# Performance work log

Measured on AMD Instinct MI355X. Metric: run time of the kernel, lower is better.

## Reference

```python
import jax, jax.numpy as jnp
import numpy as np

BETA = 0.5
N = 4096

def setup_inputs() -> dict:
    key = jax.random.key(0)
    k1, k2, k3 = jax.random.split(key, 3)
    A = jax.random.uniform(k1, (N, N), dtype=jnp.float32)
    h = jax.random.normal(k2, (N, N), dtype=jnp.float32)
    W = jax.random.normal(k3, (N, N), dtype=jnp.float32) * (1.0 / np.sqrt(N))
    return {"A": A, "h": h, "W": W}

def reference(A, h, W):
    # degrees from original A (before self-loops); D = diag(deg) + I is diagonal,
    # so torch.inverse(D) == elementwise reciprocal 1/(deg+1)
    deg = jnp.sum(A, axis=1)                       # [N]
    inv_d = 1.0 / (deg + 1.0)                      # [N]
    A_I = A + jnp.eye(A.shape[0], dtype=A.dtype)   # A += I
    # A_st = (A+I) @ diag(inv_d): scale columns
    A_st = A_I * inv_d[None, :]                    # [N,N]
    # A_st_11 = A_st @ h is dead code in the original (never used) -> skipped
    temp = BETA * h + (1.0 - BETA) * A_st          # [N,N]
    return temp @ W                                # [N,N]
```

## Files before the change

### kernel.cpp

```cpp
#include <hip/hip_runtime.h>
#include <hip/hip_bf16.h>

typedef unsigned short u16;
typedef unsigned int u32;
typedef __attribute__((ext_vector_type(8))) short bf16x8;
typedef __attribute__((ext_vector_type(4))) short s16x4;
typedef __attribute__((ext_vector_type(4))) float f32x4;

#define NN 4096

__device__ __forceinline__ u16 f2bf(float f) {
    union { float f; u32 u; } v; v.f = f;
    u32 r = v.u + 0x7fffu + ((v.u >> 16) & 1u);
    return (u16)(r >> 16);
}

__global__ void rowsum_kernel(const float* __restrict__ A, float* __restrict__ invd) {
    const int row = blockIdx.x;
    const float4* a4 = reinterpret_cast<const float4*>(A + (size_t)row * NN);
    float s = 0.f;
    #pragma unroll
    for (int i = 0; i < 4; ++i) {
        float4 v = a4[threadIdx.x + i * 256];
        s += v.x + v.y + v.z + v.w;
    }
    #pragma unroll
    for (int off = 32; off > 0; off >>= 1) s += __shfl_down(s, off, 64);
    __shared__ float ws[4];
    if ((threadIdx.x & 63) == 0) ws[threadIdx.x >> 6] = s;
    __syncthreads();
    if (threadIdx.x == 0) {
        float t = ws[0] + ws[1] + ws[2] + ws[3];
        invd[row] = 1.0f / (t + 1.0f);
    }
}

__global__ void make_temp_kernel(const float* __restrict__ A, const float* __restrict__ h,
                                 const float* __restrict__ invd, u16* __restrict__ T) {
    const size_t g = ((size_t)blockIdx.x * 256 + threadIdx.x) * 8;
    const int row = (int)(g >> 12);
    const int col = (int)(g & 4095);
    const float4* a4 = reinterpret_cast<const float4*>(A + g);
    const float4* h4 = reinterpret_cast<const float4*>(h + g);
    const float4* d4 = reinterpret_cast<const float4*>(invd + col);
    float4 a0 = a4[0], a1 = a4[1];
    float4 h0 = h4[0], h1 = h4[1];
    float4 dd0 = d4[0], dd1 = d4[1];
    float av[8] = {a0.x,a0.y,a0.z,a0.w,a1.x,a1.y,a1.z,a1.w};
    float hv[8] = {h0.x,h0.y,h0.z,h0.w,h1.x,h1.y,h1.z,h1.w};
    float dv[8] = {dd0.x,dd0.y,dd0.z,dd0.w,dd1.x,dd1.y,dd1.z,dd1.w};
    bf16x8 o;
    #pragma unroll
    for (int j = 0; j < 8; ++j) {
        float aa = av[j] + ((col + j == row) ? 1.0f : 0.0f);
        float t = 0.5f * hv[j] + 0.5f * aa * dv[j];
        o[j] = (short)f2bf(t);
    }
    *reinterpret_cast<bf16x8*>(T + g) = o;
}

__global__ void transposeW_kernel(const float* __restrict__ W, u16* __restrict__ Wt) {
    __shared__ float tile[64][65];
    const int nt = blockIdx.x & 63;
    const int kt = blockIdx.x >> 6;
    const int k0 = kt * 64, n0 = nt * 64;
    const int tr = threadIdx.x >> 4;
    const int tc = (threadIdx.x & 15) * 4;
    #pragma unroll
    for (int rr = 0; rr < 64; rr += 16) {
        float4 v = *reinterpret_cast<const float4*>(&W[(size_t)(k0 + tr + rr) * NN + n0 + tc]);
        tile[tr + rr][tc + 0] = v.x;
        tile[tr + rr][tc + 1] = v.y;
        tile[tr + rr][tc + 2] = v.z;
        tile[tr + rr][tc + 3] = v.w;
    }
    __syncthreads();
    #pragma unroll
    for (int rr = 0; rr < 64; rr += 16) {
        const int n = tr + rr;
        s16x4 o;
        #pragma unroll
        for (int j = 0; j < 4; ++j) o[j] = (short)f2bf(tile[tc + j][n]);
        *reinterpret_cast<s16x4*>(&Wt[(size_t)(n0 + n) * NN + k0 + tc]) = o;
    }
}


#define GLD16(g, l) __builtin_amdgcn_global_load_lds( \
    (const __attribute__((address_space(1))) void*)(g), \
    (__attribute__((address_space(3))) void*)(l), 16, 0, 0)

__global__ __launch_bounds__(512, 2) void gemm_kernel(
    const u16* __restrict__ Atl,
    const u16* __restrict__ Btl,
    float* __restrict__ C)
{
    __shared__ u16 SA[3][8192];
    __shared__ u16 SB[3][8192];

    const int tid  = threadIdx.x;
    const int wid  = tid >> 6;
    const int lane = tid & 63;
    const int llo  = lane & 15;
    const int lhi  = lane >> 4;
    const int wr   = wid >> 2;
    const int wc   = wid & 3;

    const int swz = ((int)blockIdx.x & 7) * 32 + ((int)blockIdx.x >> 3);
    const int bm = swz >> 4, bn = swz & 15;
    const int tileRow = bm * 256, tileCol = bn * 256;

    const int r0 = tid >> 2;
    const int kc = (((tid & 3) ^ ((r0 >> 1) & 3)) << 3);
    const size_t R128 = (size_t)128 * NN;
    const u16* gA = Atl + (size_t)(tileRow + r0) * NN + kc;
    const u16* gB = Btl + (size_t)(tileCol + r0) * NN + kc;

    #define STAGE(WB, KOFF) do { \
        GLD16(gA + (KOFF),        &SA[WB][tid * 8]); \
        GLD16(gA + R128 + (KOFF), &SA[WB][4096 + tid * 8]); \
        GLD16(gB + (KOFF),        &SB[WB][tid * 8]); \
        GLD16(gB + R128 + (KOFF), &SB[WB][4096 + tid * 8]); } while (0)

    int offA[8], offB[4];
    #pragma unroll
    for (int m = 0; m < 8; ++m) {
        const int row = wr * 128 + m * 16 + llo;
        offA[m] = row * 32 + ((lhi ^ ((row >> 1) & 3)) << 3);
    }
    #pragma unroll
    for (int n = 0; n < 4; ++n) {
        const int row = wc * 64 + n * 16 + llo;
        offB[n] = row * 32 + ((lhi ^ ((row >> 1) & 3)) << 3);
    }

    f32x4 acc[8][4];
    #pragma unroll
    for (int m = 0; m < 8; ++m)
        #pragma unroll
        for (int n = 0; n < 4; ++n)
            acc[m][n] = (f32x4){0.f, 0.f, 0.f, 0.f};

    bf16x8 aE[8], bE[4], aO[8], bO[4];

    STAGE(0, 0);
    STAGE(1, 32);
    asm volatile("s_waitcnt vmcnt(4)" ::: "memory");
    __builtin_amdgcn_s_barrier();
    asm volatile("" ::: "memory");
    #pragma unroll
    for (int m = 0; m < 8; ++m) aE[m] = *reinterpret_cast<const bf16x8*>(&SA[0][0] + offA[m]);
    #pragma unroll
    for (int n = 0; n < 4; ++n) bE[n] = *reinterpret_cast<const bf16x8*>(&SB[0][0] + offB[n]);

    int wb = 2;
    int rb = 1;
    int koff = 64;

    #define STEP(SG, VM0, RD, AC, BC, AN, BN) do { \
        if (SG) { STAGE(wb, koff); koff += 32; } \
        if (VM0) asm volatile("s_waitcnt vmcnt(0)" ::: "memory"); \
        else     asm volatile("s_waitcnt vmcnt(4)" ::: "memory"); \
        __builtin_amdgcn_s_barrier(); \
        asm volatile("" ::: "memory"); \
        const u16* rA = &SA[rb][0]; \
        const u16* rB = &SB[rb][0]; \
        if (RD) { \
            _Pragma("unroll") \
            for (int m = 0; m < 4; ++m) AN[m] = *reinterpret_cast<const bf16x8*>(rA + offA[m]); \
        } \
        __builtin_amdgcn_sched_barrier(0); \
        __builtin_amdgcn_s_setprio(1); \
        _Pragma("unroll") \
        for (int m = 0; m < 4; ++m) \
            _Pragma("unroll") \
            for (int n = 0; n < 4; ++n) \
                acc[m][n] = __builtin_amdgcn_mfma_f32_16x16x32_bf16(AC[m], BC[n], acc[m][n], 0, 0, 0); \
        __builtin_amdgcn_s_setprio(0); \
        __builtin_amdgcn_sched_barrier(0); \
        if (RD) { \
            _Pragma("unroll") \
            for (int m = 4; m < 8; ++m) AN[m] = *reinterpret_cast<const bf16x8*>(rA + offA[m]); \
            _Pragma("unroll") \
            for (int n = 0; n < 4; ++n) BN[n] = *reinterpret_cast<const bf16x8*>(rB + offB[n]); \
        } \
        __builtin_amdgcn_sched_barrier(0); \
        __builtin_amdgcn_s_setprio(1); \
        _Pragma("unroll") \
        for (int m = 4; m < 8; ++m) \
            _Pragma("unroll") \
            for (int n = 0; n < 4; ++n) \
                acc[m][n] = __builtin_amdgcn_mfma_f32_16x16x32_bf16(AC[m], BC[n], acc[m][n], 0, 0, 0); \
        __builtin_amdgcn_s_setprio(0); \
        rb = (rb == 2) ? 0 : rb + 1; \
        wb = (wb == 2) ? 0 : wb + 1; \
    } while (0)

    #pragma unroll 1
    for (int tt = 0; tt < 64; ++tt) {
        const bool sg = tt < 63;
        STEP(sg, !sg, true, aE, bE, aO, bO);
        STEP(sg, !sg && false, sg, aO, bO, aE, bE);
    }
    #undef STEP
    #undef STAGE

    #pragma unroll
    for (int m = 0; m < 8; ++m) {
        #pragma unroll
        for (int n = 0; n < 4; ++n) {
            const size_t rbase = (size_t)(tileRow + wr * 128 + m * 16 + lhi * 4) * NN
                               + tileCol + wc * 64 + n * 16 + llo;
            #pragma unroll
            for (int j = 0; j < 4; ++j)
                C[rbase + (size_t)j * NN] = acc[m][n][j];
        }
    }
}

extern "C" void kernel_launch(void* const* d_in, const int* in_sizes, int n_in,
                              void* d_out, int out_size, void* d_ws, size_t ws_size,
                              hipStream_t stream) {
    const float* A = (const float*)d_in[0];
    const float* h = (const float*)d_in[1];
    const float* W = (const float*)d_in[2];
    float* out = (float*)d_out;

    float* invd = (float*)d_ws;
    u16* temp = (u16*)((char*)d_ws + 16384);
    u16* wt   = temp + (size_t)NN * NN;

    rowsum_kernel<<<NN, 256, 0, stream>>>(A, invd);
    make_temp_kernel<<<(NN * (size_t)NN) / (256 * 8), 256, 0, stream>>>(A, h, invd, temp);
    transposeW_kernel<<<(NN / 64) * (NN / 64), 256, 0, stream>>>(W, wt);
    gemm_kernel<<<256, 512, 0, stream>>>(temp, wt, out);
}
```

Before: 179.0 us.

## Load B fragments directly from global into registers, double-buffer A with K=64 tiles

Restructures the GEMM pipeline. The B operand is no longer staged in LDS; each wave loads its B fragments straight from global memory into registers, double-buffered across steps. The A operand now uses a two-buffer LDS scheme with 64-wide K tiles and an 8-way XOR swizzle. This removes the LDS traffic and space for B and halves the number of barriers, but the A-tile reads from LDS move onto the critical path. It also relies on global-load latency for B, and wave pairs that share columns now fetch the same B data redundantly through cache.

```diff
diff --git a/kernel.cpp b/kernel.cpp
--- a/kernel.cpp
+++ b/kernel.cpp
@@ -90,13 +90,12 @@
     (const __attribute__((address_space(1))) void*)(g), \
     (__attribute__((address_space(3))) void*)(l), 16, 0, 0)
 
-__global__ __launch_bounds__(512, 2) void gemm_kernel(
+__global__ __launch_bounds__(512) void gemm_kernel(
     const u16* __restrict__ Atl,
     const u16* __restrict__ Btl,
     float* __restrict__ C)
 {
-    __shared__ u16 SA[3][8192];
-    __shared__ u16 SB[3][8192];
+    __shared__ u16 SA[2][16384];
 
     const int tid  = threadIdx.x;
     const int wid  = tid >> 6;
@@ -110,29 +109,34 @@
     const int bm = swz >> 4, bn = swz & 15;
     const int tileRow = bm * 256, tileCol = bn * 256;
 
-    const int r0 = tid >> 2;
-    const int kc = (((tid & 3) ^ ((r0 >> 1) & 3)) << 3);
-    const size_t R128 = (size_t)128 * NN;
+    const int r0 = tid >> 3;
+    const int kc = (((tid & 7) ^ (r0 & 7)) << 3);
     const u16* gA = Atl + (size_t)(tileRow + r0) * NN + kc;
-    const u16* gB = Btl + (size_t)(tileCol + r0) * NN + kc;
-
-    #define STAGE(WB, KOFF) do { \
-        GLD16(gA + (KOFF),        &SA[WB][tid * 8]); \
-        GLD16(gA + R128 + (KOFF), &SA[WB][4096 + tid * 8]); \
-        GLD16(gB + (KOFF),        &SB[WB][tid * 8]); \
-        GLD16(gB + R128 + (KOFF), &SB[WB][4096 + tid * 8]); } while (0)
-
-    int offA[8], offB[4];
+
+    #define STAGE_A(BUF, KOFF) do { \
+        _Pragma("unroll") \
+        for (int i = 0; i < 4; ++i) \
+            GLD16(gA + (size_t)(i * 64) * NN + (KOFF), &SA[BUF][i * 4096 + tid * 8]); \
+    } while (0)
+
+    int offA[8];
     #pragma unroll
     for (int m = 0; m < 8; ++m) {
         const int row = wr * 128 + m * 16 + llo;
-        offA[m] = row * 32 + ((lhi ^ ((row >> 1) & 3)) << 3);
-    }
-    #pragma unroll
-    for (int n = 0; n < 4; ++n) {
-        const int row = wc * 64 + n * 16 + llo;
-        offB[n] = row * 32 + ((lhi ^ ((row >> 1) & 3)) << 3);
-    }
+        offA[m] = row * 64 + ((lhi ^ (row & 7)) << 3);
+    }
+
+    const u16* gBr[4];
+    #pragma unroll
+    for (int n = 0; n < 4; ++n)
+        gBr[n] = Btl + (size_t)(tileCol + wc * 64 + n * 16 + llo) * NN + lhi * 8;
+
+    #define BLOAD(SET, KB) do { \
+        _Pragma("unroll") \
+        for (int n = 0; n < 4; ++n) { \
+            SET[n][0] = *reinterpret_cast<const bf16x8*>(gBr[n] + (KB)); \
+            SET[n][1] = *reinterpret_cast<const bf16x8*>(gBr[n] + (KB) + 32); \
+        } } while (0)
 
     f32x4 acc[8][4];
     #pragma unroll
@@ -141,69 +145,55 @@
         for (int n = 0; n < 4; ++n)
             acc[m][n] = (f32x4){0.f, 0.f, 0.f, 0.f};
 
-    bf16x8 aE[8], bE[4], aO[8], bO[4];
-
-    STAGE(0, 0);
-    STAGE(1, 32);
-    asm volatile("s_waitcnt vmcnt(4)" ::: "memory");
+    bf16x8 bE[4][2], bO[4][2];
+
+    STAGE_A(0, 0);
+    BLOAD(bE, 0);
+    asm volatile("s_waitcnt vmcnt(0)" ::: "memory");
     __builtin_amdgcn_s_barrier();
     asm volatile("" ::: "memory");
-    #pragma unroll
-    for (int m = 0; m < 8; ++m) aE[m] = *reinterpret_cast<const bf16x8*>(&SA[0][0] + offA[m]);
-    #pragma unroll
-    for (int n = 0; n < 4; ++n) bE[n] = *reinterpret_cast<const bf16x8*>(&SB[0][0] + offB[n]);
-
-    int wb = 2;
-    int rb = 1;
-    int koff = 64;
-
-    #define STEP(SG, VM0, RD, AC, BC, AN, BN) do { \
-        if (SG) { STAGE(wb, koff); koff += 32; } \
-        if (VM0) asm volatile("s_waitcnt vmcnt(0)" ::: "memory"); \
-        else     asm volatile("s_waitcnt vmcnt(4)" ::: "memory"); \
-        __builtin_amdgcn_s_barrier(); \
-        asm volatile("" ::: "memory"); \
-        const u16* rA = &SA[rb][0]; \
-        const u16* rB = &SB[rb][0]; \
-        if (RD) { \
-            _Pragma("unroll") \
-            for (int m = 0; m < 4; ++m) AN[m] = *reinterpret_cast<const bf16x8*>(rA + offA[m]); \
-        } \
+
+    #define STEP(T, BC, BNX) do { \
+        const int t_ = (T); \
+        const bool nlast_ = t_ < 63; \
+        if (nlast_) STAGE_A((t_ + 1) & 1, (t_ + 1) * 64); \
         __builtin_amdgcn_sched_barrier(0); \
+        const u16* sA = &SA[t_ & 1][0]; \
+        bf16x8 af[8]; \
+        _Pragma("unroll") \
+        for (int m = 0; m < 8; ++m) af[m] = *reinterpret_cast<const bf16x8*>(sA + offA[m]); \
         __builtin_amdgcn_s_setprio(1); \
         _Pragma("unroll") \
-        for (int m = 0; m < 4; ++m) \
+        for (int m = 0; m < 8; ++m) \
             _Pragma("unroll") \
             for (int n = 0; n < 4; ++n) \
-                acc[m][n] = __builtin_amdgcn_mfma_f32_16x16x32_bf16(AC[m], BC[n], acc[m][n], 0, 0, 0); \
+                acc[m][n] = __builtin_amdgcn_mfma_f32_16x16x32_bf16(af[m], BC[n][0], acc[m][n], 0, 0, 0); \
         __builtin_amdgcn_s_setprio(0); \
-        __builtin_amdgcn_sched_barrier(0); \
-        if (RD) { \
-            _Pragma("unroll") \
-            for (int m = 4; m < 8; ++m) AN[m] = *reinterpret_cast<const bf16x8*>(rA + offA[m]); \
-            _Pragma("unroll") \
-            for (int n = 0; n < 4; ++n) BN[n] = *reinterpret_cast<const bf16x8*>(rB + offB[n]); \
-        } \
-        __builtin_amdgcn_sched_barrier(0); \
+        if (nlast_) BLOAD(BNX, (t_ + 1) * 64); \
+        _Pragma("unroll") \
+        for (int m = 0; m < 8; ++m) af[m] = *reinterpret_cast<const bf16x8*>(sA + (offA[m] ^ 32)); \
         __builtin_amdgcn_s_setprio(1); \
         _Pragma("unroll") \
-        for (int m = 4; m < 8; ++m) \
+        for (int m = 0; m < 8; ++m) \
             _Pragma("unroll") \
             for (int n = 0; n < 4; ++n) \
-                acc[m][n] = __builtin_amdgcn_mfma_f32_16x16x32_bf16(AC[m], BC[n], acc[m][n], 0, 0, 0); \
+                acc[m][n] = __builtin_amdgcn_mfma_f32_16x16x32_bf16(af[m], BC[n][1], acc[m][n], 0, 0, 0); \
         __builtin_amdgcn_s_setprio(0); \
-        rb = (rb == 2) ? 0 : rb + 1; \
-        wb = (wb == 2) ? 0 : wb + 1; \
+        if (nlast_) { \
+            asm volatile("s_waitcnt vmcnt(0)" ::: "memory"); \
+            __builtin_amdgcn_s_barrier(); \
+            asm volatile("" ::: "memory"); \
+        } \
     } while (0)
 
     #pragma unroll 1
-    for (int tt = 0; tt < 64; ++tt) {
-        const bool sg = tt < 63;
-        STEP(sg, !sg, true, aE, bE, aO, bO);
-        STEP(sg, !sg && false, sg, aO, bO, aE, bE);
+    for (int tt = 0; tt < 32; ++tt) {
+        STEP(2 * tt,     bE, bO);
+        STEP(2 * tt + 1, bO, bE);
     }
     #undef STEP
-    #undef STAGE
+    #undef BLOAD
+    #undef STAGE_A
 
     #pragma unroll
     for (int m = 0; m < 8; ++m) {
```

Result: slower. 363.8 us (+103.3%).
